# Performance work log

Hardware: AMD Instinct MI355X
Metric: run time of the kernel (lower is better)

The kernel has to match this reference:

```python
import jax, jax.numpy as jnp
import numpy as np
from jax import lax

# PSTConv constants (match init_kwargs)
R = 0.5            # ball-query radius
K = 32             # neighbors per anchor
SPATIAL_STRIDE = 2
TK = 3             # temporal kernel size (odd)
TSTRIDE = 1        # temporal stride
PAD = (1, 1)       # temporal padding, 'zeros' mode
MID = 128
OUT = 256


def setup_inputs() -> dict:
    key = jax.random.key(0)
    k1, k2, k3, k4, k5 = jax.random.split(key, 5)
    B, L, N, C = 8, 6, 2048, 64
    xyzs = jax.random.uniform(k1, (B, L, N, 3), dtype=jnp.float32)
    features = jax.random.normal(k2, (B, L, C, N), dtype=jnp.float32)
    # kaiming_uniform with size=[mid, in+3, 1, 1]: bound = 1/sqrt(in_planes+3)
    b = 1.0 / np.sqrt(C + 3)
    w_d = jax.random.uniform(k3, (MID, 3), minval=-b, maxval=b, dtype=jnp.float32)
    w_f = jax.random.uniform(k4, (MID, C), minval=-b, maxval=b, dtype=jnp.float32)
    bt = 1.0 / np.sqrt(TK * MID)
    w_t = jax.random.uniform(k5, (OUT, TK * MID), minval=-bt, maxval=bt, dtype=jnp.float32)
    return {"xyzs": xyzs, "features": features, "w_d": w_d, "w_f": w_f, "w_t": w_t}


def _fps(xyz, m):
    # furthest point sampling on [N,3]; CUDA kernel starts from index 0
    N = xyz.shape[0]
    def step(carry, _):
        dists, far = carry
        d = jnp.sum((xyz - xyz[far]) ** 2, axis=-1)
        dists = jnp.minimum(dists, d)
        nxt = jnp.argmax(dists).astype(jnp.int32)
        return (dists, nxt), far
    init = (jnp.full((N,), 1e10, dtype=xyz.dtype), jnp.int32(0))
    _, idx = lax.scan(step, init, None, length=m)
    return idx  # [m] int32


def _ball_query(nbr_xyz, anchor_xyz):
    # nbr_xyz [B,N,3], anchor_xyz [B,M,3] -> [B,M,K] int32 indices into N
    # Semantics of pointnet2 ball_query: first K points (in index order) within
    # radius R; slots past the count are filled with the first found index
    # (0 if no point is in range).
    N = nbr_xyz.shape[1]
    d2 = jnp.sum((anchor_xyz[:, :, None, :] - nbr_xyz[:, None, :, :]) ** 2, axis=-1)  # [B,M,N]
    vals = jnp.where(d2 < R * R, jnp.arange(N, dtype=jnp.int32), jnp.int32(N))
    neg_top, _ = lax.top_k(-vals, K)          # K smallest indices, ascending
    idx = -neg_top                            # [B,M,K]
    first = idx[..., :1]
    fill = jnp.where(first < N, first, 0)
    return jnp.where(idx < N, idx, fill)


def _group(feat, idx):
    # feat [B,C,N], idx [B,M,K] -> [B,C,M,K]
    return jax.vmap(lambda f, i: f[:, i])(feat, idx)


def reference(xyzs, features, w_d, w_f, w_t):
    B, L, N, _ = xyzs.shape
    M = N // SPATIAL_STRIDE
    rad = TK // 2
    # zero temporal padding
    zx = jnp.zeros((B, 1, N, 3), xyzs.dtype)
    zf = jnp.zeros((B, 1, features.shape[2], N), features.dtype)
    xp = jnp.concatenate([zx] * PAD[0] + [xyzs] + [zx] * PAD[1], axis=1)
    fp = jnp.concatenate([zf] * PAD[0] + [features] + [zf] * PAD[1], axis=1)
    Lp = L + PAD[0] + PAD[1]

    new_xyzs, new_feats = [], []
    fps_b = jax.vmap(lambda x: _fps(x, M))
    for t in range(rad, Lp - rad, TSTRIDE):
        xyz_t = xp[:, t]                                   # [B,N,3]
        aidx = fps_b(xyz_t)                                # [B,M]
        anchor = jnp.take_along_axis(xyz_t, aidx[:, :, None], axis=1)  # [B,M,3]
        anchor_c = jnp.transpose(anchor, (0, 2, 1))[:, :, :, None]     # [B,3,M,1]
        sfs = []
        for i in range(t - rad, t + rad + 1):
            idx = _ball_query(xp[:, i], anchor)            # [B,M,K]
            g_xyz = _group(jnp.transpose(xp[:, i], (0, 2, 1)), idx)    # [B,3,M,K]
            disp = g_xyz - anchor_c
            d = jnp.einsum('oc,bcmk->bomk', w_d, disp)     # [B,MID,M,K]
            g_f = _group(fp[:, i], idx)                    # [B,C,M,K]
            f = jnp.einsum('oc,bcmk->bomk', w_f, g_f)
            sfs.append(jnp.max(f + d, axis=-1))            # [B,MID,M]
        sf = jax.nn.relu(jnp.concatenate(sfs, axis=1))     # [B,TK*MID,M]
        new_feats.append(jnp.einsum('oc,bcm->bom', w_t, sf))
        new_xyzs.append(anchor)
    return jnp.stack(new_xyzs, axis=1), jnp.stack(new_feats, axis=1)
```

## Files before the change

### kernel.cpp

```cpp
#include <hip/hip_runtime.h>

#define BATCH 8
#define LFRM  6
#define NP    2048
#define MP    1024
#define CIN   64
#define MIDC  128
#define OUTC  256
#define TKM   384
#define KNN   32
#define RAD2  0.25f

#define FPS_BLOCKS (BATCH * LFRM)
#define FT_BLOCKS  (BATCH * LFRM * (NP / 64))
#define WFS 132

typedef float f2 __attribute__((ext_vector_type(2)));
typedef float f32x4 __attribute__((ext_vector_type(4)));
typedef _Float16 f16x8 __attribute__((ext_vector_type(8)));
typedef _Float16 f16x4 __attribute__((ext_vector_type(4)));

union SharedU {
  struct {
    float4 pts[NP];
    unsigned long long wk[2][4];
  } fps;
  struct {
    float ftile[CIN][64];
    float wfT[CIN][WFS];
    float xt[64], yt[64], zt[64];
    float wdl[MIDC * 3];
  } ft;
};

__device__ __forceinline__ uint64_t kmax64(uint64_t a, uint64_t b) {
  return a > b ? a : b;
}
template <int CTRL>
__device__ __forceinline__ uint64_t key_dpp(uint64_t k) {
  int lo = __builtin_amdgcn_update_dpp((int)(uint32_t)k, (int)(uint32_t)k,
                                       CTRL, 0xF, 0xF, false);
  int hi = __builtin_amdgcn_update_dpp((int)(uint32_t)(k >> 32),
                                       (int)(uint32_t)(k >> 32),
                                       CTRL, 0xF, 0xF, false);
  return ((uint64_t)(uint32_t)hi << 32) | (uint32_t)lo;
}

__device__ __forceinline__ void fps_path(const float* __restrict__ xyzs,
                                         float* __restrict__ out_xyz,
                                         SharedU* sh) {
#pragma clang fp contract(off)
  const int bt = blockIdx.x;
  const int tid = threadIdx.x;
  const int lane = tid & 63, wv = tid >> 6;
  const float* src = xyzs + (size_t)bt * NP * 3;

  for (int q = tid; q < NP; q += 256)
    sh->fps.pts[q] = make_float4(src[q * 3 + 0], src[q * 3 + 1], src[q * 3 + 2], 0.f);
  __syncthreads();

  f2 px[4], py[4], pz[4], dist[4];
#pragma unroll
  for (int u = 0; u < 4; ++u) {
    float4 a = sh->fps.pts[(wv * 8 + 2 * u) * 64 + lane];
    float4 b = sh->fps.pts[(wv * 8 + 2 * u + 1) * 64 + lane];
    px[u] = f2{a.x, b.x};
    py[u] = f2{a.y, b.y};
    pz[u] = f2{a.z, b.z};
    dist[u] = f2{1e10f, 1e10f};
  }

  float4 p0 = sh->fps.pts[0];
  float fx = p0.x, fy = p0.y, fz = p0.z;
  float* dst = out_xyz + (size_t)bt * MP * 3;

  for (int it = 0; it < MP; ++it) {
    if (tid == 0) {
      dst[it * 3 + 0] = fx;
      dst[it * 3 + 1] = fy;
      dst[it * 3 + 2] = fz;
    }
    const f2 fx2 = {fx, fx}, fy2 = {fy, fy}, fz2 = {fz, fz};
    float bv = -1.0f;
    int bsu = 0;
#pragma unroll
    for (int u = 0; u < 4; ++u) {
      f2 dx = px[u] - fx2;
      f2 dy = py[u] - fy2;
      f2 dz = pz[u] - fz2;
      f2 m = dx * dx;
      m = m + dy * dy;
      m = m + dz * dz;
      f2 nd = __builtin_elementwise_min(dist[u], m);
      dist[u] = nd;
      bool cx = nd.x > bv;
      bv = cx ? nd.x : bv;
      bsu = cx ? 2 * u : bsu;
      bool cy = nd.y > bv;
      bv = cy ? nd.y : bv;
      bsu = cy ? 2 * u + 1 : bsu;
    }
    const uint32_t p = (uint32_t)(((wv * 8 + bsu) << 6) | lane);
    uint64_t key = ((uint64_t)__float_as_uint(bv) << 32) | (uint32_t)(~p);
    key = kmax64(key, key_dpp<0x121>(key));
    key = kmax64(key, key_dpp<0x122>(key));
    key = kmax64(key, key_dpp<0x124>(key));
    key = kmax64(key, key_dpp<0x128>(key));
    key = kmax64(key, key_dpp<0x142>(key));
    key = kmax64(key, key_dpp<0x143>(key));

    const int par = it & 1;
    if (lane == 63) sh->fps.wk[par][wv] = key;
    __syncthreads();
    uint64_t k0 = kmax64(sh->fps.wk[par][0], sh->fps.wk[par][1]);
    uint64_t k1 = kmax64(sh->fps.wk[par][2], sh->fps.wk[par][3]);
    uint64_t kg = kmax64(k0, k1);
    const uint32_t wp = ~(uint32_t)kg;
    float4 w = sh->fps.pts[wp];
    fx = w.x; fy = w.y; fz = w.z;
  }
}

__device__ __forceinline__ void ftrans_path(const float* __restrict__ features,
                                            const float* __restrict__ w_f,
                                            const float* __restrict__ w_d,
                                            const float* __restrict__ xyzs,
                                            float* __restrict__ G,
                                            SharedU* sh) {
  const int blk = blockIdx.x - FPS_BLOCKS;
  const int ntile = blk & 31;
  const int bl = blk >> 5;
  const int tid = threadIdx.x;

  const float* fsrc = features + (size_t)bl * CIN * NP + (size_t)ntile * 64;
  for (int idx = tid; idx < CIN * 64; idx += 256) {
    int c = idx >> 6, n = idx & 63;
    sh->ft.ftile[c][n] = fsrc[(size_t)c * NP + n];
  }
  for (int idx = tid; idx < CIN * MIDC; idx += 256) {
    int c = idx & 63, o = idx >> 6;
    sh->ft.wfT[c][o] = w_f[o * CIN + c];
  }
  if (tid < 64) {
    const float* xs = xyzs + ((size_t)bl * NP + (size_t)ntile * 64 + tid) * 3;
    sh->ft.xt[tid] = xs[0];
    sh->ft.yt[tid] = xs[1];
    sh->ft.zt[tid] = xs[2];
  }
  for (int idx = tid; idx < MIDC * 3; idx += 256) sh->ft.wdl[idx] = w_d[idx];
  __syncthreads();

  const int op = tid & 31;
  const int ng = tid >> 5;
  const int ob = op * 4;
  const int nb = ng * 8;

  float acc[4][8];
#pragma unroll
  for (int oo = 0; oo < 4; ++oo) {
    const float w0 = sh->ft.wdl[(ob + oo) * 3 + 0];
    const float w1 = sh->ft.wdl[(ob + oo) * 3 + 1];
    const float w2 = sh->ft.wdl[(ob + oo) * 3 + 2];
#pragma unroll
    for (int j = 0; j < 8; ++j)
      acc[oo][j] = w0 * sh->ft.xt[nb + j] + w1 * sh->ft.yt[nb + j] +
                   w2 * sh->ft.zt[nb + j];
  }

#pragma unroll 4
  for (int c = 0; c < CIN; ++c) {
    const float4 wq = *(const float4*)&sh->ft.wfT[c][ob];
    const float4 fA = *(const float4*)&sh->ft.ftile[c][nb];
    const float4 fB = *(const float4*)&sh->ft.ftile[c][nb + 4];
    const float wo[4] = {wq.x, wq.y, wq.z, wq.w};
    const float fv[8] = {fA.x, fA.y, fA.z, fA.w, fB.x, fB.y, fB.z, fB.w};
#pragma unroll
    for (int oo = 0; oo < 4; ++oo)
#pragma unroll
      for (int j = 0; j < 8; ++j)
        acc[oo][j] += wo[oo] * fv[j];
  }

  float* dstp = G + ((size_t)bl * NP + (size_t)ntile * 64) * MIDC;
#pragma unroll
  for (int j = 0; j < 8; ++j) {
    float4 v = make_float4(acc[0][j], acc[1][j], acc[2][j], acc[3][j]);
    *(float4*)&dstp[(size_t)(nb + j) * MIDC + ob] = v;
  }
}

__global__ __launch_bounds__(256, 1) void fps_ftrans_kernel(
    const float* __restrict__ xyzs, const float* __restrict__ features,
    const float* __restrict__ w_f, const float* __restrict__ w_d,
    float* __restrict__ out_xyz, float* __restrict__ G) {
  __shared__ SharedU sh;
  if (blockIdx.x < FPS_BLOCKS) {
    fps_path(xyzs, out_xyz, &sh);
    return;
  }
  ftrans_path(features, w_f, w_d, xyzs, G, &sh);
}

#define PSTR 392

__global__ __launch_bounds__(256) void pst_main(const float* __restrict__ xyzs,
                                                const float* __restrict__ w_d,
                                                const float* __restrict__ w_t,
                                                const float* __restrict__ G,
                                                const float* __restrict__ anchors,
                                                float* __restrict__ out_feat) {
  __shared__ float pxyz[NP * 3];
  __shared__ _Float16 sfp16[32][PSTR];
  __shared__ unsigned short nidx[32][KNN];
  __shared__ float anc[32][3];

  const int blk = blockIdx.x;
  const int mt = blk & 31;
  const int bt = blk >> 5;
  const int b = bt / LFRM;
  const int t = bt % LFRM + 1;
  const int tid = threadIdx.x;

  const float* asrc = anchors + ((size_t)bt * MP + (size_t)mt * 32) * 3;
  if (tid < 96) anc[tid / 3][tid % 3] = asrc[tid];
  __syncthreads();

  const int al = tid >> 3;
  const int j = tid & 7;
  const float ax = anc[al][0], ay = anc[al][1], az = anc[al][2];

  float wda[16];
#pragma unroll
  for (int c4 = 0; c4 < 4; ++c4)
#pragma unroll
    for (int r = 0; r < 4; ++r) {
      int o = c4 * 32 + j * 4 + r;
      wda[c4 * 4 + r] = w_d[o * 3 + 0] * ax + w_d[o * 3 + 1] * ay +
                        w_d[o * 3 + 2] * az;
    }

  const int lane = tid & 63, wv = tid >> 6;

  for (int ii = 0; ii < 3; ++ii) {
    const int i = t - 1 + ii;
    float mg[16];
#pragma unroll
    for (int u = 0; u < 16; ++u) mg[u] = 0.f;

    if (i != 0 && i != LFRM + 1) {
      const int f2i = i - 1;
      const float* fxyz = xyzs + (size_t)(b * LFRM + f2i) * NP * 3;
      __syncthreads();
      for (int q = tid; q < NP * 3; q += 256) pxyz[q] = fxyz[q];
      __syncthreads();

      for (int aa = 0; aa < 8; ++aa) {
        const int a = wv * 8 + aa;
        const float qx = anc[a][0], qy = anc[a][1], qz = anc[a][2];
        int total = 0;
        int fillidx = 0;
        for (int ch = 0; ch < NP / 64; ++ch) {
          const int p = ch * 64 + lane;
          float d2;
          {
#pragma clang fp contract(off)
            float dx = qx - pxyz[p * 3 + 0];
            float dy = qy - pxyz[p * 3 + 1];
            float dz = qz - pxyz[p * 3 + 2];
            d2 = dx * dx + dy * dy + dz * dz;
          }
          const bool inb = d2 < RAD2;
          const unsigned long long mk = __ballot(inb);
          if (mk != 0ull && total == 0)
            fillidx = ch * 64 + (int)__builtin_ctzll(mk);
          const int before = (int)__builtin_popcountll(mk & ((1ull << lane) - 1ull));
          const int slot = total + before;
          if (inb && slot < KNN) nidx[a][slot] = (unsigned short)p;
          total += (int)__builtin_popcountll(mk);
          if (total >= KNN) break;
        }
        const int nf = total < KNN ? total : KNN;
        if (lane < KNN - nf) nidx[a][nf + lane] = (unsigned short)fillidx;
      }
      __syncthreads();

      const float* gf = G + (size_t)(b * LFRM + f2i) * NP * MIDC;
#pragma unroll
      for (int u = 0; u < 16; ++u) mg[u] = -1e30f;
      for (int k = 0; k < KNN; ++k) {
        const int p = nidx[al][k];
        const float4* row = (const float4*)(gf + (size_t)p * MIDC);
#pragma unroll
        for (int c4 = 0; c4 < 4; ++c4) {
          float4 v = row[c4 * 8 + j];
          mg[c4 * 4 + 0] = fmaxf(mg[c4 * 4 + 0], v.x);
          mg[c4 * 4 + 1] = fmaxf(mg[c4 * 4 + 1], v.y);
          mg[c4 * 4 + 2] = fmaxf(mg[c4 * 4 + 2], v.z);
          mg[c4 * 4 + 3] = fmaxf(mg[c4 * 4 + 3], v.w);
        }
      }
    }

#pragma unroll
    for (int c4 = 0; c4 < 4; ++c4) {
      f16x4 h;
#pragma unroll
      for (int r = 0; r < 4; ++r)
        h[r] = (_Float16)fmaxf(mg[c4 * 4 + r] - wda[c4 * 4 + r], 0.f);
      *(f16x4*)&sfp16[al][ii * MIDC + c4 * 32 + j * 4] = h;
    }
  }
  __syncthreads();

  const int l16 = lane & 15, lq = lane >> 4;
  f32x4 accm[4][2];
#pragma unroll
  for (int q = 0; q < 4; ++q)
#pragma unroll
    for (int n2 = 0; n2 < 2; ++n2) accm[q][n2] = f32x4{0.f, 0.f, 0.f, 0.f};

  for (int kc = 0; kc < TKM / 32; ++kc) {
    f16x8 bfr[2];
#pragma unroll
    for (int n2 = 0; n2 < 2; ++n2)
      bfr[n2] = *(const f16x8*)&sfp16[n2 * 16 + l16][kc * 32 + lq * 8];
#pragma unroll
    for (int q = 0; q < 4; ++q) {
      const int row = (wv * 4 + q) * 16 + l16;
      const float4* ap = (const float4*)(w_t + (size_t)row * TKM + kc * 32 + lq * 8);
      float4 a0 = ap[0], a1 = ap[1];
      f16x8 afr;
      afr[0] = (_Float16)a0.x; afr[1] = (_Float16)a0.y;
      afr[2] = (_Float16)a0.z; afr[3] = (_Float16)a0.w;
      afr[4] = (_Float16)a1.x; afr[5] = (_Float16)a1.y;
      afr[6] = (_Float16)a1.z; afr[7] = (_Float16)a1.w;
      accm[q][0] = __builtin_amdgcn_mfma_f32_16x16x32_f16(afr, bfr[0], accm[q][0], 0, 0, 0);
      accm[q][1] = __builtin_amdgcn_mfma_f32_16x16x32_f16(afr, bfr[1], accm[q][1], 0, 0, 0);
    }
  }

  float* ob = out_feat + (size_t)bt * OUTC * MP + (size_t)mt * 32;
#pragma unroll
  for (int q = 0; q < 4; ++q) {
    const int orow = (wv * 4 + q) * 16 + lq * 4;
#pragma unroll
    for (int n2 = 0; n2 < 2; ++n2)
#pragma unroll
      for (int r = 0; r < 4; ++r)
        ob[(size_t)(orow + r) * MP + n2 * 16 + l16] = accm[q][n2][r];
  }
}

extern "C" void kernel_launch(void* const* d_in, const int* in_sizes, int n_in,
                              void* d_out, int out_size, void* d_ws, size_t ws_size,
                              hipStream_t stream) {
  const float* xyzs = (const float*)d_in[0];
  const float* features = (const float*)d_in[1];
  const float* w_d = (const float*)d_in[2];
  const float* w_f = (const float*)d_in[3];
  const float* w_t = (const float*)d_in[4];

  float* out = (float*)d_out;
  float* out_xyz = out;
  float* out_feat = out + (size_t)BATCH * LFRM * MP * 3;
  float* G = (float*)d_ws;

  hipLaunchKernelGGL(fps_ftrans_kernel, dim3(FPS_BLOCKS + FT_BLOCKS), dim3(256),
                     0, stream, xyzs, features, w_f, w_d, out_xyz, G);
  hipLaunchKernelGGL(pst_main, dim3(BATCH * LFRM * (MP / 32)), dim3(256), 0,
                     stream, xyzs, w_d, w_t, G, out_xyz, out_feat);
}
```

Baseline: 618.2 us.

## Alias point and feature LDS buffers, drop gather barrier, rework FPS wave reduction

In the main kernel the point-coordinate buffer and the fp16 feature tile now share one LDS union, which roughly halves per-block shared memory so more blocks can be resident. Per-frame results are kept in registers until the end, so the barrier between ball query and gather can be dropped. That is safe only because each wave reads only the neighbour lists it wrote itself. The gather loop is partially unrolled. In the FPS kernel the last two row-broadcast DPP steps of the argmax reduction are replaced by a ds_swizzle and a shfl_xor, and the result is read from lane 0. This adds register pressure from holding 12 f16x4 values per thread.

```diff
diff --git a/kernel.cpp b/kernel.cpp
--- a/kernel.cpp
+++ b/kernel.cpp
@@ -43,6 +43,16 @@
   int hi = __builtin_amdgcn_update_dpp((int)(uint32_t)(k >> 32),
                                        (int)(uint32_t)(k >> 32),
                                        CTRL, 0xF, 0xF, false);
+  return ((uint64_t)(uint32_t)hi << 32) | (uint32_t)lo;
+}
+__device__ __forceinline__ uint64_t key_swz16(uint64_t k) {
+  int lo = __builtin_amdgcn_ds_swizzle((int)(uint32_t)k, 0x401F);
+  int hi = __builtin_amdgcn_ds_swizzle((int)(uint32_t)(k >> 32), 0x401F);
+  return ((uint64_t)(uint32_t)hi << 32) | (uint32_t)lo;
+}
+__device__ __forceinline__ uint64_t key_x32(uint64_t k) {
+  int lo = __shfl_xor((int)(uint32_t)k, 32);
+  int hi = __shfl_xor((int)(uint32_t)(k >> 32), 32);
   return ((uint64_t)(uint32_t)hi << 32) | (uint32_t)lo;
 }
 
@@ -106,11 +116,11 @@
     key = kmax64(key, key_dpp<0x122>(key));
     key = kmax64(key, key_dpp<0x124>(key));
     key = kmax64(key, key_dpp<0x128>(key));
-    key = kmax64(key, key_dpp<0x142>(key));
-    key = kmax64(key, key_dpp<0x143>(key));
+    key = kmax64(key, key_swz16(key));
+    key = kmax64(key, key_x32(key));
 
     const int par = it & 1;
-    if (lane == 63) sh->fps.wk[par][wv] = key;
+    if (lane == 0) sh->fps.wk[par][wv] = key;
     __syncthreads();
     uint64_t k0 = kmax64(sh->fps.wk[par][0], sh->fps.wk[par][1]);
     uint64_t k1 = kmax64(sh->fps.wk[par][2], sh->fps.wk[par][3]);
@@ -209,8 +219,10 @@
                                                 const float* __restrict__ G,
                                                 const float* __restrict__ anchors,
                                                 float* __restrict__ out_feat) {
-  __shared__ float pxyz[NP * 3];
-  __shared__ _Float16 sfp16[32][PSTR];
+  __shared__ union {
+    float pxyz[NP * 3];
+    _Float16 sf[32][PSTR];
+  } u;
   __shared__ unsigned short nidx[32][KNN];
   __shared__ float anc[32][3];
 
@@ -241,17 +253,26 @@
 
   const int lane = tid & 63, wv = tid >> 6;
 
+  f16x4 hreg[3][4];
+
+#pragma unroll
   for (int ii = 0; ii < 3; ++ii) {
     const int i = t - 1 + ii;
-    float mg[16];
-#pragma unroll
-    for (int u = 0; u < 16; ++u) mg[u] = 0.f;
-
-    if (i != 0 && i != LFRM + 1) {
+
+    if (i == 0 || i == LFRM + 1) {
+#pragma unroll
+      for (int c4 = 0; c4 < 4; ++c4) {
+        f16x4 h;
+#pragma unroll
+        for (int r = 0; r < 4; ++r)
+          h[r] = (_Float16)fmaxf(-wda[c4 * 4 + r], 0.f);
+        hreg[ii][c4] = h;
+      }
+    } else {
       const int f2i = i - 1;
       const float* fxyz = xyzs + (size_t)(b * LFRM + f2i) * NP * 3;
       __syncthreads();
-      for (int q = tid; q < NP * 3; q += 256) pxyz[q] = fxyz[q];
+      for (int q = tid; q < NP * 3; q += 256) u.pxyz[q] = fxyz[q];
       __syncthreads();
 
       for (int aa = 0; aa < 8; ++aa) {
@@ -264,9 +285,9 @@
           float d2;
           {
 #pragma clang fp contract(off)
-            float dx = qx - pxyz[p * 3 + 0];
-            float dy = qy - pxyz[p * 3 + 1];
-            float dz = qz - pxyz[p * 3 + 2];
+            float dx = qx - u.pxyz[p * 3 + 0];
+            float dy = qy - u.pxyz[p * 3 + 1];
+            float dz = qz - u.pxyz[p * 3 + 2];
             d2 = dx * dx + dy * dy + dz * dz;
           }
           const bool inb = d2 < RAD2;
@@ -282,34 +303,41 @@
         const int nf = total < KNN ? total : KNN;
         if (lane < KNN - nf) nidx[a][nf + lane] = (unsigned short)fillidx;
       }
-      __syncthreads();
 
       const float* gf = G + (size_t)(b * LFRM + f2i) * NP * MIDC;
-#pragma unroll
-      for (int u = 0; u < 16; ++u) mg[u] = -1e30f;
+      float mg[16];
+#pragma unroll
+      for (int uq = 0; uq < 16; ++uq) mg[uq] = -1e30f;
+#pragma unroll 4
       for (int k = 0; k < KNN; ++k) {
         const int p = nidx[al][k];
-        const float4* row = (const float4*)(gf + (size_t)p * MIDC);
+        const float* rowp = gf + (size_t)p * MIDC + j * 4;
 #pragma unroll
         for (int c4 = 0; c4 < 4; ++c4) {
-          float4 v = row[c4 * 8 + j];
+          float4 v = *(const float4*)(rowp + c4 * 32);
           mg[c4 * 4 + 0] = fmaxf(mg[c4 * 4 + 0], v.x);
           mg[c4 * 4 + 1] = fmaxf(mg[c4 * 4 + 1], v.y);
           mg[c4 * 4 + 2] = fmaxf(mg[c4 * 4 + 2], v.z);
           mg[c4 * 4 + 3] = fmaxf(mg[c4 * 4 + 3], v.w);
         }
       }
+#pragma unroll
+      for (int c4 = 0; c4 < 4; ++c4) {
+        f16x4 h;
+#pragma unroll
+        for (int r = 0; r < 4; ++r)
+          h[r] = (_Float16)fmaxf(mg[c4 * 4 + r] - wda[c4 * 4 + r], 0.f);
+        hreg[ii][c4] = h;
+      }
     }
-
-#pragma unroll
-    for (int c4 = 0; c4 < 4; ++c4) {
-      f16x4 h;
-#pragma unroll
-      for (int r = 0; r < 4; ++r)
-        h[r] = (_Float16)fmaxf(mg[c4 * 4 + r] - wda[c4 * 4 + r], 0.f);
-      *(f16x4*)&sfp16[al][ii * MIDC + c4 * 32 + j * 4] = h;
-    }
-  }
+  }
+
+  __syncthreads();
+#pragma unroll
+  for (int ii = 0; ii < 3; ++ii)
+#pragma unroll
+    for (int c4 = 0; c4 < 4; ++c4)
+      *(f16x4*)&u.sf[al][ii * MIDC + c4 * 32 + j * 4] = hreg[ii][c4];
   __syncthreads();
 
   const int l16 = lane & 15, lq = lane >> 4;
@@ -323,7 +351,7 @@
     f16x8 bfr[2];
 #pragma unroll
     for (int n2 = 0; n2 < 2; ++n2)
-      bfr[n2] = *(const f16x8*)&sfp16[n2 * 16 + l16][kc * 32 + lq * 8];
+      bfr[n2] = *(const f16x8*)&u.sf[n2 * 16 + l16][kc * 32 + lq * 8];
 #pragma unroll
     for (int q = 0; q < 4; ++q) {
       const int row = (wv * 4 + q) * 16 + l16;
```

New measurement: 648.7 us. +4.9%, slower.
